# Kernel optimization log

Hardware: AMD Instinct MI355X
Metric: run time of the kernel (lower is better)

Reference implementation:

```python
import jax, jax.numpy as jnp
import numpy as np

LR = 0.001
TAU = 1000.0


def setup_inputs() -> dict:
    key = jax.random.key(0)
    k1, k2 = jax.random.split(key)
    B, IN, OUT = 8192, 4096, 4096
    x = jax.random.normal(k1, (B, IN), dtype=jnp.float32)
    weight = jax.random.normal(k2, (OUT, IN), dtype=jnp.float32) * 0.1
    threshold = jnp.zeros((OUT,), dtype=jnp.float32)
    return {"x": x, "weight": weight, "threshold": threshold}


def reference(x, weight, threshold):
    # output = x @ W.T  -> (B, out)
    output = jnp.matmul(x, weight.T)

    # BCM sliding-threshold EMA (torch uses output.detach())
    activity = jnp.mean(jax.lax.stop_gradient(output), axis=0)  # (out,)
    new_threshold = threshold + (activity ** 2 - threshold) / TAU

    # Hebbian update: torch builds (B, out, in) outer products then means over B;
    # equivalent efficient form: post.T @ pre / B (single GEMM).
    post = jax.lax.stop_gradient(jnp.maximum(output - new_threshold, 0.0))  # (B, out)
    B = x.shape[0]
    delta_w = (LR / B) * jnp.einsum('bo,bi->oi', post, x)
    new_weight = weight + delta_w

    # Original returns (output, threshold-after-update); we also expose the
    # updated weight (the in-place .data side effect) for verification.
    return output, new_threshold, new_weight
```

## Files before the change

### kernel.cpp

```cpp
#include <hip/hip_runtime.h>
#include <hip/hip_bf16.h>


typedef __attribute__((ext_vector_type(8))) short   bf16x8;
typedef __attribute__((ext_vector_type(4))) float   f32x4;

#define ASG __attribute__((address_space(1)))
#define ASL __attribute__((address_space(3)))

__device__ __forceinline__ void gload16(const void* g, void* l) {
    __builtin_amdgcn_global_load_lds((const ASG void*)g, (ASL void*)l, 16, 0, 0);
}

__device__ __forceinline__ unsigned short f2bf(float x) {
    union { float f; unsigned u; } v; v.f = x;
    unsigned r = v.u;
    r += 0x7fffu + ((r >> 16) & 1u);
    return (unsigned short)(r >> 16);
}
__device__ __forceinline__ float bf2f(unsigned short u) {
    union { unsigned u; float f; } v; v.u = ((unsigned)u) << 16;
    return v.f;
}

__global__ __launch_bounds__(256) void k_cvt_split(const float* __restrict__ src,
                                                   unsigned short* __restrict__ hi,
                                                   unsigned short* __restrict__ lo,
                                                   int n4) {
    int i = blockIdx.x * blockDim.x + threadIdx.x;
    int stride = gridDim.x * blockDim.x;
    for (; i < n4; i += stride) {
        float4 v = reinterpret_cast<const float4*>(src)[i];
        ushort4 h, l;
        h.x = f2bf(v.x); l.x = f2bf(v.x - bf2f(h.x));
        h.y = f2bf(v.y); l.y = f2bf(v.y - bf2f(h.y));
        h.z = f2bf(v.z); l.z = f2bf(v.z - bf2f(h.z));
        h.w = f2bf(v.w); l.w = f2bf(v.w - bf2f(h.w));
        reinterpret_cast<ushort4*>(hi)[i] = h;
        reinterpret_cast<ushort4*>(lo)[i] = l;
    }
}

__global__ __launch_bounds__(256) void k_prep_x(const float* __restrict__ x,
                                                unsigned short* __restrict__ hi,
                                                unsigned short* __restrict__ lo,
                                                unsigned short* __restrict__ xT) {
    __shared__ unsigned short tile[64][65];
    const int b0 = blockIdx.y * 64, i0 = blockIdx.x * 64;
#pragma unroll
    for (int it = 0; it < 16; ++it) {
        int idx = it * 256 + threadIdx.x;
        int r = idx >> 6, c = idx & 63;
        float v = x[(size_t)(b0 + r) * 4096 + i0 + c];
        unsigned short h = f2bf(v);
        unsigned short l = f2bf(v - bf2f(h));
        hi[(size_t)(b0 + r) * 4096 + i0 + c] = h;
        lo[(size_t)(b0 + r) * 4096 + i0 + c] = l;
        tile[r][c] = h;
    }
    __syncthreads();
#pragma unroll
    for (int it = 0; it < 16; ++it) {
        int idx = it * 256 + threadIdx.x;
        int r = idx >> 6, c = idx & 63;
        xT[(size_t)(i0 + r) * 8192 + b0 + c] = tile[c][r];
    }
}

__global__ __launch_bounds__(512, 2) void k_gemm1(const unsigned short* __restrict__ Ah,
                                                  const unsigned short* __restrict__ Al,
                                                  const unsigned short* __restrict__ Bh,
                                                  const unsigned short* __restrict__ Bl,
                                                  float* __restrict__ C,
                                                  float* __restrict__ acc_act) {
    __shared__ unsigned short sm[3 * 24576];
    const int t = threadIdx.x, lane = t & 63, ln15 = lane & 15, l16 = lane >> 4;
    const int wid = t >> 6, wm = wid >> 2, wn = wid & 3;
    const int nwg = gridDim.x, bid = blockIdx.x;
    const int wg  = (bid & 7) * (nwg >> 3) + (bid >> 3);
    const int bm = wg >> 5, bn = wg & 31;
    const int arow0 = bm * 256, brow0 = bn * 128;

    const unsigned short* gsrc[6];
    int ldso[6];
#pragma unroll
    for (int j = 0; j < 6; ++j) {
        const int c = j * 512 + t;
        if (c < 1024)      { int cc = c;        int row = cc >> 2, chk = (cc & 3) ^ ((row >> 1) & 3); gsrc[j] = Ah + (size_t)(arow0 + row) * 4096 + chk * 8; ldso[j] = cc * 8; }
        else if (c < 2048) { int cc = c - 1024; int row = cc >> 2, chk = (cc & 3) ^ ((row >> 1) & 3); gsrc[j] = Al + (size_t)(arow0 + row) * 4096 + chk * 8; ldso[j] = 8192 + cc * 8; }
        else if (c < 2560) { int cc = c - 2048; int row = cc >> 2, chk = (cc & 3) ^ ((row >> 1) & 3); gsrc[j] = Bh + (size_t)(brow0 + row) * 4096 + chk * 8; ldso[j] = 16384 + cc * 8; }
        else               { int cc = c - 2560; int row = cc >> 2, chk = (cc & 3) ^ ((row >> 1) & 3); gsrc[j] = Bl + (size_t)(brow0 + row) * 4096 + chk * 8; ldso[j] = 20480 + cc * 8; }
    }

    int aoh[8], aol[8], boh[2], bol[2];
#pragma unroll
    for (int mi = 0; mi < 8; ++mi) {
        const int r = wm * 128 + mi * 16 + ln15;
        const int sw = (l16 ^ ((r >> 1) & 3)) * 8;
        aoh[mi] = r * 32 + sw; aol[mi] = 8192 + r * 32 + sw;
    }
#pragma unroll
    for (int ni = 0; ni < 2; ++ni) {
        const int r = wn * 32 + ni * 16 + ln15;
        const int sw = (l16 ^ ((r >> 1) & 3)) * 8;
        boh[ni] = 16384 + r * 32 + sw; bol[ni] = 20480 + r * 32 + sw;
    }

    f32x4 acc[8][2];
#pragma unroll
    for (int mi = 0; mi < 8; ++mi)
#pragma unroll
        for (int ni = 0; ni < 2; ++ni) acc[mi][ni] = (f32x4){0.f, 0.f, 0.f, 0.f};

#pragma unroll
    for (int j = 0; j < 6; ++j) gload16(gsrc[j], sm + ldso[j]);
#pragma unroll
    for (int j = 0; j < 6; ++j) gload16(gsrc[j] + 32, sm + 24576 + ldso[j]);

    int scur = 0, snxt = 2;
    for (int kt = 0; kt < 128; ++kt) {
        asm volatile("s_waitcnt vmcnt(6)" ::: "memory");
        __builtin_amdgcn_s_barrier();
        asm volatile("" ::: "memory");
        const unsigned short* rb = sm + scur * 24576;
        bf16x8 vah[8], val[8], vbh[2], vbl[2];
#pragma unroll
        for (int mi = 0; mi < 8; ++mi) { vah[mi] = *(const bf16x8*)(rb + aoh[mi]); val[mi] = *(const bf16x8*)(rb + aol[mi]); }
#pragma unroll
        for (int ni = 0; ni < 2; ++ni) { vbh[ni] = *(const bf16x8*)(rb + boh[ni]); vbl[ni] = *(const bf16x8*)(rb + bol[ni]); }
        {
            const size_t ko = (size_t)((kt + 2 < 128) ? kt + 2 : 127) * 32;
            unsigned short* sb = sm + snxt * 24576;
#pragma unroll
            for (int j = 0; j < 6; ++j) gload16(gsrc[j] + ko, sb + ldso[j]);
        }
        __builtin_amdgcn_s_setprio(1);
#pragma unroll
        for (int mi = 0; mi < 8; ++mi)
#pragma unroll
            for (int ni = 0; ni < 2; ++ni) {
                acc[mi][ni] = __builtin_amdgcn_mfma_f32_16x16x32_bf16(vah[mi], vbh[ni], acc[mi][ni], 0, 0, 0);
                acc[mi][ni] = __builtin_amdgcn_mfma_f32_16x16x32_bf16(vah[mi], vbl[ni], acc[mi][ni], 0, 0, 0);
                acc[mi][ni] = __builtin_amdgcn_mfma_f32_16x16x32_bf16(val[mi], vbh[ni], acc[mi][ni], 0, 0, 0);
            }
        __builtin_amdgcn_s_setprio(0);
        scur = (scur == 2) ? 0 : scur + 1;
        snxt = (snxt == 2) ? 0 : snxt + 1;
    }
    asm volatile("s_waitcnt vmcnt(0)" ::: "memory");

    const int row0 = bm * 256 + wm * 128, col0 = bn * 128 + wn * 32;
    float cs0 = 0.f, cs1 = 0.f;
#pragma unroll
    for (int mi = 0; mi < 8; ++mi)
#pragma unroll
        for (int j = 0; j < 4; ++j) {
            const int row = row0 + mi * 16 + l16 * 4 + j;
            C[(size_t)row * 4096 + col0 + ln15]      = acc[mi][0][j];
            C[(size_t)row * 4096 + col0 + 16 + ln15] = acc[mi][1][j];
            cs0 += acc[mi][0][j]; cs1 += acc[mi][1][j];
        }
    cs0 += __shfl_xor(cs0, 16, 64); cs0 += __shfl_xor(cs0, 32, 64);
    cs1 += __shfl_xor(cs1, 16, 64); cs1 += __shfl_xor(cs1, 32, 64);
    if (l16 == 0) {
        atomicAdd(&acc_act[col0 + ln15], cs0);
        atomicAdd(&acc_act[col0 + 16 + ln15], cs1);
    }
}

__global__ __launch_bounds__(512, 2) void k_gemm2(const unsigned short* __restrict__ A,
                                                  const unsigned short* __restrict__ Bx,
                                                  const float* __restrict__ Wf,
                                                  float* __restrict__ Wout, float scale) {
    __shared__ unsigned short sm[3 * 24576];
    const int t = threadIdx.x, lane = t & 63, ln15 = lane & 15, l16 = lane >> 4;
    const int wid = t >> 6, wm = wid >> 2, wn = wid & 3;
    const int nwg = gridDim.x, bid = blockIdx.x;
    const int wg  = (bid & 7) * (nwg >> 3) + (bid >> 3);
    const int bm = wg >> 5, bn = wg & 31;
    const int arow0 = bm * 256, brow0 = bn * 128;

    const unsigned short* gsrc[6];
    int ldso[6];
#pragma unroll
    for (int j = 0; j < 6; ++j) {
        const int c = j * 512 + t;
        if (c < 2048) { int row = c >> 3, chk = (c & 7) ^ (row & 7); gsrc[j] = A + (size_t)(arow0 + row) * 8192 + chk * 8; ldso[j] = c * 8; }
        else { int cc = c - 2048; int row = cc >> 3, chk = (cc & 7) ^ (row & 7); gsrc[j] = Bx + (size_t)(brow0 + row) * 8192 + chk * 8; ldso[j] = 16384 + cc * 8; }
    }

    int ao0[8], ao1[8], bo0[2], bo1[2];
#pragma unroll
    for (int mi = 0; mi < 8; ++mi) {
        const int r = wm * 128 + mi * 16 + ln15;
        ao0[mi] = r * 64 + ((l16 ^ (r & 7)) * 8);
        ao1[mi] = r * 64 + (((4 + l16) ^ (r & 7)) * 8);
    }
#pragma unroll
    for (int ni = 0; ni < 2; ++ni) {
        const int r = wn * 32 + ni * 16 + ln15;
        bo0[ni] = 16384 + r * 64 + ((l16 ^ (r & 7)) * 8);
        bo1[ni] = 16384 + r * 64 + (((4 + l16) ^ (r & 7)) * 8);
    }

    f32x4 acc[8][2];
#pragma unroll
    for (int mi = 0; mi < 8; ++mi)
#pragma unroll
        for (int ni = 0; ni < 2; ++ni) acc[mi][ni] = (f32x4){0.f, 0.f, 0.f, 0.f};

#pragma unroll
    for (int j = 0; j < 6; ++j) gload16(gsrc[j], sm + ldso[j]);
#pragma unroll
    for (int j = 0; j < 6; ++j) gload16(gsrc[j] + 64, sm + 24576 + ldso[j]);

    int scur = 0, snxt = 2;
    for (int kt = 0; kt < 128; ++kt) {
        asm volatile("s_waitcnt vmcnt(6)" ::: "memory");
        __builtin_amdgcn_s_barrier();
        asm volatile("" ::: "memory");
        const unsigned short* rb = sm + scur * 24576;
        bf16x8 va[8], vb[2];
#pragma unroll
        for (int mi = 0; mi < 8; ++mi) va[mi] = *(const bf16x8*)(rb + ao0[mi]);
#pragma unroll
        for (int ni = 0; ni < 2; ++ni) vb[ni] = *(const bf16x8*)(rb + bo0[ni]);
        { const size_t ko = (size_t)((kt + 2 < 128) ? kt + 2 : 127) * 64;
          unsigned short* sb = sm + snxt * 24576;
#pragma unroll
          for (int j = 0; j < 6; ++j) gload16(gsrc[j] + ko, sb + ldso[j]);
        }
        __builtin_amdgcn_s_setprio(1);
#pragma unroll
        for (int mi = 0; mi < 8; ++mi)
#pragma unroll
            for (int ni = 0; ni < 2; ++ni)
                acc[mi][ni] = __builtin_amdgcn_mfma_f32_16x16x32_bf16(va[mi], vb[ni], acc[mi][ni], 0, 0, 0);
        __builtin_amdgcn_s_setprio(0);
#pragma unroll
        for (int mi = 0; mi < 8; ++mi) va[mi] = *(const bf16x8*)(rb + ao1[mi]);
#pragma unroll
        for (int ni = 0; ni < 2; ++ni) vb[ni] = *(const bf16x8*)(rb + bo1[ni]);
        __builtin_amdgcn_s_setprio(1);
#pragma unroll
        for (int mi = 0; mi < 8; ++mi)
#pragma unroll
            for (int ni = 0; ni < 2; ++ni)
                acc[mi][ni] = __builtin_amdgcn_mfma_f32_16x16x32_bf16(va[mi], vb[ni], acc[mi][ni], 0, 0, 0);
        __builtin_amdgcn_s_setprio(0);
        scur = (scur == 2) ? 0 : scur + 1;
        snxt = (snxt == 2) ? 0 : snxt + 1;
    }
    asm volatile("s_waitcnt vmcnt(0)" ::: "memory");

    const int row0 = bm * 256 + wm * 128, col0 = bn * 128 + wn * 32;
#pragma unroll
    for (int mi = 0; mi < 8; ++mi)
#pragma unroll
        for (int j = 0; j < 4; ++j) {
            const int row = row0 + mi * 16 + l16 * 4 + j;
            const size_t i0 = (size_t)row * 4096 + col0 + ln15;
            const size_t i1 = i0 + 16;
            Wout[i0] = Wf[i0] + scale * acc[mi][0][j];
            Wout[i1] = Wf[i1] + scale * acc[mi][1][j];
        }
}

__global__ __launch_bounds__(256) void k_thr(const float* __restrict__ acc,
                                             const float* __restrict__ thr_in,
                                             float* __restrict__ thr_out) {
    const int o = blockIdx.x * 256 + threadIdx.x;
    const float act = acc[o] * (1.0f / 8192.0f);
    const float t0  = thr_in[o];
    thr_out[o] = t0 + (act * act - t0) / 1000.0f;
}

__global__ __launch_bounds__(256) void k_postT(const float* __restrict__ out,
                                               const float* __restrict__ thr,
                                               unsigned short* __restrict__ postT) {
    __shared__ unsigned short tile[64][65];
    __shared__ float sthr[64];
    const int b0 = blockIdx.y * 64, o0 = blockIdx.x * 64;
    if (threadIdx.x < 64) sthr[threadIdx.x] = thr[o0 + threadIdx.x];
    __syncthreads();
#pragma unroll
    for (int it = 0; it < 16; ++it) {
        int idx = it * 256 + threadIdx.x;
        int r = idx >> 6, c = idx & 63;
        float v = out[(size_t)(b0 + r) * 4096 + o0 + c] - sthr[c];
        tile[r][c] = f2bf(v > 0.f ? v : 0.f);
    }
    __syncthreads();
#pragma unroll
    for (int it = 0; it < 16; ++it) {
        int idx = it * 256 + threadIdx.x;
        int r = idx >> 6, c = idx & 63;
        postT[(size_t)(o0 + r) * 8192 + b0 + c] = tile[c][r];
    }
}

extern "C" void kernel_launch(void* const* d_in, const int* in_sizes, int n_in,
                              void* d_out, int out_size, void* d_ws, size_t ws_size,
                              hipStream_t stream) {
    const float* x   = (const float*)d_in[0];
    const float* w   = (const float*)d_in[1];
    const float* thr = (const float*)d_in[2];
    const int B = 8192, IN = 4096, OUT = 4096;

    float* out_y   = (float*)d_out;
    float* out_thr = out_y + (size_t)B * OUT;
    float* out_w   = out_thr + OUT;

    char* ws = (char*)d_ws;
    float* acc_act       = (float*)ws;
    unsigned short* x_hi = (unsigned short*)(ws + 65536);
    unsigned short* x_lo = x_hi + (size_t)B * IN;
    unsigned short* w_hi = x_lo + (size_t)B * IN;
    unsigned short* w_lo = w_hi + (size_t)OUT * IN;
    unsigned short* xT   = w_lo + (size_t)OUT * IN;
    unsigned short* postT = x_lo;
    (void)ws_size;

    hipMemsetAsync(acc_act, 0, OUT * sizeof(float), stream);

    k_prep_x<<<dim3(IN / 64, B / 64), 256, 0, stream>>>(x, x_hi, x_lo, xT);
    k_cvt_split<<<2048, 256, 0, stream>>>(w, w_hi, w_lo, OUT * IN / 4);

    k_gemm1<<<1024, 512, 0, stream>>>(x_hi, x_lo, w_hi, w_lo, out_y, acc_act);

    k_thr<<<OUT / 256, 256, 0, stream>>>(acc_act, thr, out_thr);

    k_postT<<<dim3(OUT / 64, B / 64), 256, 0, stream>>>(out_y, out_thr, postT);

    k_gemm2<<<512, 512, 0, stream>>>(postT, xT, w, out_w, (float)(0.001 / 8192.0));
}
```

Measured before the change: 1.375 ms.

## Reshape GEMM warp tiles to 64x64 and double-buffer LDS fragments in registers

Both GEMM kernels change each wave's tile from 128x32 to 64x64, which cuts the number of LDS fragment reads per MFMA. The main loop is unrolled by two with register double-buffering, so the next k-slice's LDS reads and global prefetch overlap the current slice's MFMAs. All three LDS stages are now prefetched up front. The second fragment buffer raises VGPR pressure, which risks spills or lower occupancy under the existing launch bounds.

```diff
diff --git a/kernel.cpp b/kernel.cpp
--- a/kernel.cpp
+++ b/kernel.cpp
@@ -67,6 +67,46 @@
     }
 }
 
+
+__device__ __forceinline__ void g1_stage(const unsigned short* const (&gsrc)[6],
+                                         const int (&ldso)[6],
+                                         unsigned short* sb, int ko) {
+#pragma unroll
+    for (int j = 0; j < 6; ++j) gload16(gsrc[j] + ko, sb + ldso[j]);
+}
+
+__device__ __forceinline__ void g1_read(const unsigned short* rb,
+                                        const int (&aoh)[4], const int (&aol)[4],
+                                        const int (&boh)[4], const int (&bol)[4],
+                                        bf16x8 (&Ah)[4], bf16x8 (&Al)[4],
+                                        bf16x8 (&Bh)[4], bf16x8 (&Bl)[4]) {
+#pragma unroll
+    for (int i = 0; i < 4; ++i) {
+        Ah[i] = *(const bf16x8*)(rb + aoh[i]);
+        Al[i] = *(const bf16x8*)(rb + aol[i]);
+    }
+#pragma unroll
+    for (int i = 0; i < 4; ++i) {
+        Bh[i] = *(const bf16x8*)(rb + boh[i]);
+        Bl[i] = *(const bf16x8*)(rb + bol[i]);
+    }
+}
+
+__device__ __forceinline__ void g1_mfma(const bf16x8 (&Ah)[4], const bf16x8 (&Al)[4],
+                                        const bf16x8 (&Bh)[4], const bf16x8 (&Bl)[4],
+                                        f32x4 (&acc)[4][4]) {
+    __builtin_amdgcn_s_setprio(1);
+#pragma unroll
+    for (int mi = 0; mi < 4; ++mi)
+#pragma unroll
+        for (int ni = 0; ni < 4; ++ni) {
+            acc[mi][ni] = __builtin_amdgcn_mfma_f32_16x16x32_bf16(Ah[mi], Bh[ni], acc[mi][ni], 0, 0, 0);
+            acc[mi][ni] = __builtin_amdgcn_mfma_f32_16x16x32_bf16(Ah[mi], Bl[ni], acc[mi][ni], 0, 0, 0);
+            acc[mi][ni] = __builtin_amdgcn_mfma_f32_16x16x32_bf16(Al[mi], Bh[ni], acc[mi][ni], 0, 0, 0);
+        }
+    __builtin_amdgcn_s_setprio(0);
+}
+
 __global__ __launch_bounds__(512, 2) void k_gemm1(const unsigned short* __restrict__ Ah,
                                                   const unsigned short* __restrict__ Al,
                                                   const unsigned short* __restrict__ Bh,
@@ -75,7 +115,7 @@
                                                   float* __restrict__ acc_act) {
     __shared__ unsigned short sm[3 * 24576];
     const int t = threadIdx.x, lane = t & 63, ln15 = lane & 15, l16 = lane >> 4;
-    const int wid = t >> 6, wm = wid >> 2, wn = wid & 3;
+    const int wid = t >> 6, wm = wid >> 1, wn = wid & 1;
     const int nwg = gridDim.x, bid = blockIdx.x;
     const int wg  = (bid & 7) * (nwg >> 3) + (bid >> 3);
     const int bm = wg >> 5, bn = wg & 31;
@@ -92,80 +132,128 @@
         else               { int cc = c - 2560; int row = cc >> 2, chk = (cc & 3) ^ ((row >> 1) & 3); gsrc[j] = Bl + (size_t)(brow0 + row) * 4096 + chk * 8; ldso[j] = 20480 + cc * 8; }
     }
 
-    int aoh[8], aol[8], boh[2], bol[2];
-#pragma unroll
-    for (int mi = 0; mi < 8; ++mi) {
-        const int r = wm * 128 + mi * 16 + ln15;
+    int aoh[4], aol[4], boh[4], bol[4];
+#pragma unroll
+    for (int mi = 0; mi < 4; ++mi) {
+        const int r = wm * 64 + mi * 16 + ln15;
         const int sw = (l16 ^ ((r >> 1) & 3)) * 8;
         aoh[mi] = r * 32 + sw; aol[mi] = 8192 + r * 32 + sw;
     }
 #pragma unroll
-    for (int ni = 0; ni < 2; ++ni) {
-        const int r = wn * 32 + ni * 16 + ln15;
+    for (int ni = 0; ni < 4; ++ni) {
+        const int r = wn * 64 + ni * 16 + ln15;
         const int sw = (l16 ^ ((r >> 1) & 3)) * 8;
         boh[ni] = 16384 + r * 32 + sw; bol[ni] = 20480 + r * 32 + sw;
     }
 
-    f32x4 acc[8][2];
-#pragma unroll
-    for (int mi = 0; mi < 8; ++mi)
-#pragma unroll
-        for (int ni = 0; ni < 2; ++ni) acc[mi][ni] = (f32x4){0.f, 0.f, 0.f, 0.f};
-
-#pragma unroll
-    for (int j = 0; j < 6; ++j) gload16(gsrc[j], sm + ldso[j]);
-#pragma unroll
-    for (int j = 0; j < 6; ++j) gload16(gsrc[j] + 32, sm + 24576 + ldso[j]);
-
-    int scur = 0, snxt = 2;
-    for (int kt = 0; kt < 128; ++kt) {
+    f32x4 acc[4][4];
+#pragma unroll
+    for (int i = 0; i < 4; ++i)
+#pragma unroll
+        for (int j = 0; j < 4; ++j) acc[i][j] = (f32x4){0.f, 0.f, 0.f, 0.f};
+
+    bf16x8 A0h[4], A0l[4], B0h[4], B0l[4];
+    bf16x8 A1h[4], A1l[4], B1h[4], B1l[4];
+
+    g1_stage(gsrc, ldso, sm, 0);
+    g1_stage(gsrc, ldso, sm + 24576, 32);
+    g1_stage(gsrc, ldso, sm + 2 * 24576, 64);
+    asm volatile("s_waitcnt vmcnt(12)" ::: "memory");
+    __builtin_amdgcn_s_barrier();
+    g1_read(sm, aoh, aol, boh, bol, A0h, A0l, B0h, B0l);
+    asm volatile("s_waitcnt lgkmcnt(0)" ::: "memory");
+    __builtin_amdgcn_sched_barrier(0);
+
+    int sRead = 1, sStage = 0;
+#pragma unroll 1
+    for (int i = 0; i < 64; ++i) {
         asm volatile("s_waitcnt vmcnt(6)" ::: "memory");
         __builtin_amdgcn_s_barrier();
-        asm volatile("" ::: "memory");
-        const unsigned short* rb = sm + scur * 24576;
-        bf16x8 vah[8], val[8], vbh[2], vbl[2];
-#pragma unroll
-        for (int mi = 0; mi < 8; ++mi) { vah[mi] = *(const bf16x8*)(rb + aoh[mi]); val[mi] = *(const bf16x8*)(rb + aol[mi]); }
-#pragma unroll
-        for (int ni = 0; ni < 2; ++ni) { vbh[ni] = *(const bf16x8*)(rb + boh[ni]); vbl[ni] = *(const bf16x8*)(rb + bol[ni]); }
-        {
-            const size_t ko = (size_t)((kt + 2 < 128) ? kt + 2 : 127) * 32;
-            unsigned short* sb = sm + snxt * 24576;
-#pragma unroll
-            for (int j = 0; j < 6; ++j) gload16(gsrc[j] + ko, sb + ldso[j]);
-        }
-        __builtin_amdgcn_s_setprio(1);
-#pragma unroll
-        for (int mi = 0; mi < 8; ++mi)
-#pragma unroll
-            for (int ni = 0; ni < 2; ++ni) {
-                acc[mi][ni] = __builtin_amdgcn_mfma_f32_16x16x32_bf16(vah[mi], vbh[ni], acc[mi][ni], 0, 0, 0);
-                acc[mi][ni] = __builtin_amdgcn_mfma_f32_16x16x32_bf16(vah[mi], vbl[ni], acc[mi][ni], 0, 0, 0);
-                acc[mi][ni] = __builtin_amdgcn_mfma_f32_16x16x32_bf16(val[mi], vbh[ni], acc[mi][ni], 0, 0, 0);
+        g1_read(sm + sRead * 24576, aoh, aol, boh, bol, A1h, A1l, B1h, B1l);
+        { int kst = 2 * i + 3; if (kst > 127) kst = 127;
+          g1_stage(gsrc, ldso, sm + sStage * 24576, kst * 32); }
+        g1_mfma(A0h, A0l, B0h, B0l, acc);
+        asm volatile("s_waitcnt lgkmcnt(0)" ::: "memory");
+        __builtin_amdgcn_sched_barrier(0);
+        sRead = (sRead == 2) ? 0 : sRead + 1;
+        sStage = (sStage == 2) ? 0 : sStage + 1;
+        asm volatile("s_waitcnt vmcnt(6)" ::: "memory");
+        __builtin_amdgcn_s_barrier();
+        g1_read(sm + sRead * 24576, aoh, aol, boh, bol, A0h, A0l, B0h, B0l);
+        { int kst = 2 * i + 4; if (kst > 127) kst = 127;
+          g1_stage(gsrc, ldso, sm + sStage * 24576, kst * 32); }
+        g1_mfma(A1h, A1l, B1h, B1l, acc);
+        asm volatile("s_waitcnt lgkmcnt(0)" ::: "memory");
+        __builtin_amdgcn_sched_barrier(0);
+        sRead = (sRead == 2) ? 0 : sRead + 1;
+        sStage = (sStage == 2) ? 0 : sStage + 1;
+    }
+    asm volatile("s_waitcnt vmcnt(0)" ::: "memory");
+
+    const int row0 = bm * 256 + wm * 64, col0 = bn * 128 + wn * 64;
+    float cs[4] = {0.f, 0.f, 0.f, 0.f};
+#pragma unroll
+    for (int mi = 0; mi < 4; ++mi)
+#pragma unroll
+        for (int ni = 0; ni < 4; ++ni)
+#pragma unroll
+            for (int j = 0; j < 4; ++j) {
+                const int row = row0 + mi * 16 + l16 * 4 + j;
+                C[(size_t)row * 4096 + col0 + ni * 16 + ln15] = acc[mi][ni][j];
+                cs[ni] += acc[mi][ni][j];
             }
-        __builtin_amdgcn_s_setprio(0);
-        scur = (scur == 2) ? 0 : scur + 1;
-        snxt = (snxt == 2) ? 0 : snxt + 1;
-    }
-    asm volatile("s_waitcnt vmcnt(0)" ::: "memory");
-
-    const int row0 = bm * 256 + wm * 128, col0 = bn * 128 + wn * 32;
-    float cs0 = 0.f, cs1 = 0.f;
-#pragma unroll
-    for (int mi = 0; mi < 8; ++mi)
-#pragma unroll
-        for (int j = 0; j < 4; ++j) {
-            const int row = row0 + mi * 16 + l16 * 4 + j;
-            C[(size_t)row * 4096 + col0 + ln15]      = acc[mi][0][j];
-            C[(size_t)row * 4096 + col0 + 16 + ln15] = acc[mi][1][j];
-            cs0 += acc[mi][0][j]; cs1 += acc[mi][1][j];
-        }
-    cs0 += __shfl_xor(cs0, 16, 64); cs0 += __shfl_xor(cs0, 32, 64);
-    cs1 += __shfl_xor(cs1, 16, 64); cs1 += __shfl_xor(cs1, 32, 64);
+#pragma unroll
+    for (int ni = 0; ni < 4; ++ni) {
+        cs[ni] += __shfl_xor(cs[ni], 16, 64);
+        cs[ni] += __shfl_xor(cs[ni], 32, 64);
+    }
     if (l16 == 0) {
-        atomicAdd(&acc_act[col0 + ln15], cs0);
-        atomicAdd(&acc_act[col0 + 16 + ln15], cs1);
-    }
+#pragma unroll
+        for (int ni = 0; ni < 4; ++ni)
+            atomicAdd(&acc_act[col0 + ni * 16 + ln15], cs[ni]);
+    }
+}
+
+
+__device__ __forceinline__ void g2_stage(const unsigned short* const (&gsrc)[6],
+                                         const int (&ldso)[6],
+                                         unsigned short* sb, int ko) {
+#pragma unroll
+    for (int j = 0; j < 6; ++j) gload16(gsrc[j] + ko, sb + ldso[j]);
+}
+
+__device__ __forceinline__ void g2_read(const unsigned short* rb,
+                                        const int (&ao0)[4], const int (&ao1)[4],
+                                        const int (&bo0)[4], const int (&bo1)[4],
+                                        bf16x8 (&A0)[4], bf16x8 (&A1)[4],
+                                        bf16x8 (&B0)[4], bf16x8 (&B1)[4]) {
+#pragma unroll
+    for (int i = 0; i < 4; ++i) {
+        A0[i] = *(const bf16x8*)(rb + ao0[i]);
+        A1[i] = *(const bf16x8*)(rb + ao1[i]);
+    }
+#pragma unroll
+    for (int i = 0; i < 4; ++i) {
+        B0[i] = *(const bf16x8*)(rb + bo0[i]);
+        B1[i] = *(const bf16x8*)(rb + bo1[i]);
+    }
+}
+
+__device__ __forceinline__ void g2_mfma(const bf16x8 (&A0)[4], const bf16x8 (&A1)[4],
+                                        const bf16x8 (&B0)[4], const bf16x8 (&B1)[4],
+                                        f32x4 (&acc)[4][4]) {
+    __builtin_amdgcn_s_setprio(1);
+#pragma unroll
+    for (int mi = 0; mi < 4; ++mi)
+#pragma unroll
+        for (int ni = 0; ni < 4; ++ni)
+            acc[mi][ni] = __builtin_amdgcn_mfma_f32_16x16x32_bf16(A0[mi], B0[ni], acc[mi][ni], 0, 0, 0);
+#pragma unroll
+    for (int mi = 0; mi < 4; ++mi)
+#pragma unroll
+        for (int ni = 0; ni < 4; ++ni)
+            acc[mi][ni] = __builtin_amdgcn_mfma_f32_16x16x32_bf16(A1[mi], B1[ni], acc[mi][ni], 0, 0, 0);
+    __builtin_amdgcn_s_setprio(0);
 }
 
 __global__ __launch_bounds__(512, 2) void k_gemm2(const unsigned short* __restrict__ A,
@@ -174,7 +262,7 @@
                                                   float* __restrict__ Wout, float scale) {
     __shared__ unsigned short sm[3 * 24576];
     const int t = threadIdx.x, lane = t & 63, ln15 = lane & 15, l16 = lane >> 4;
-    const int wid = t >> 6, wm = wid >> 2, wn = wid & 3;
+    const int wid = t >> 6, wm = wid >> 1, wn = wid & 1;
     const int nwg = gridDim.x, bid = blockIdx.x;
     const int wg  = (bid & 7) * (nwg >> 3) + (bid >> 3);
     const int bm = wg >> 5, bn = wg & 31;
@@ -189,81 +277,76 @@
         else { int cc = c - 2048; int row = cc >> 3, chk = (cc & 7) ^ (row & 7); gsrc[j] = Bx + (size_t)(brow0 + row) * 8192 + chk * 8; ldso[j] = 16384 + cc * 8; }
     }
 
-    int ao0[8], ao1[8], bo0[2], bo1[2];
-#pragma unroll
-    for (int mi = 0; mi < 8; ++mi) {
-        const int r = wm * 128 + mi * 16 + ln15;
+    int ao0[4], ao1[4], bo0[4], bo1[4];
+#pragma unroll
+    for (int mi = 0; mi < 4; ++mi) {
+        const int r = wm * 64 + mi * 16 + ln15;
         ao0[mi] = r * 64 + ((l16 ^ (r & 7)) * 8);
         ao1[mi] = r * 64 + (((4 + l16) ^ (r & 7)) * 8);
     }
 #pragma unroll
-    for (int ni = 0; ni < 2; ++ni) {
-        const int r = wn * 32 + ni * 16 + ln15;
+    for (int ni = 0; ni < 4; ++ni) {
+        const int r = wn * 64 + ni * 16 + ln15;
         bo0[ni] = 16384 + r * 64 + ((l16 ^ (r & 7)) * 8);
         bo1[ni] = 16384 + r * 64 + (((4 + l16) ^ (r & 7)) * 8);
     }
 
-    f32x4 acc[8][2];
-#pragma unroll
-    for (int mi = 0; mi < 8; ++mi)
-#pragma unroll
-        for (int ni = 0; ni < 2; ++ni) acc[mi][ni] = (f32x4){0.f, 0.f, 0.f, 0.f};
-
-#pragma unroll
-    for (int j = 0; j < 6; ++j) gload16(gsrc[j], sm + ldso[j]);
-#pragma unroll
-    for (int j = 0; j < 6; ++j) gload16(gsrc[j] + 64, sm + 24576 + ldso[j]);
-
-    int scur = 0, snxt = 2;
-    for (int kt = 0; kt < 128; ++kt) {
+    f32x4 acc[4][4];
+#pragma unroll
+    for (int i = 0; i < 4; ++i)
+#pragma unroll
+        for (int j = 0; j < 4; ++j) acc[i][j] = (f32x4){0.f, 0.f, 0.f, 0.f};
+
+    bf16x8 A0k0[4], A0k1[4], B0k0[4], B0k1[4];
+    bf16x8 A1k0[4], A1k1[4], B1k0[4], B1k1[4];
+
+    g2_stage(gsrc, ldso, sm, 0);
+    g2_stage(gsrc, ldso, sm + 24576, 64);
+    g2_stage(gsrc, ldso, sm + 2 * 24576, 128);
+    asm volatile("s_waitcnt vmcnt(12)" ::: "memory");
+    __builtin_amdgcn_s_barrier();
+    g2_read(sm, ao0, ao1, bo0, bo1, A0k0, A0k1, B0k0, B0k1);
+    asm volatile("s_waitcnt lgkmcnt(0)" ::: "memory");
+    __builtin_amdgcn_sched_barrier(0);
+
+    int sRead = 1, sStage = 0;
+#pragma unroll 1
+    for (int i = 0; i < 64; ++i) {
         asm volatile("s_waitcnt vmcnt(6)" ::: "memory");
         __builtin_amdgcn_s_barrier();
-        asm volatile("" ::: "memory");
-        const unsigned short* rb = sm + scur * 24576;
-        bf16x8 va[8], vb[2];
-#pragma unroll
-        for (int mi = 0; mi < 8; ++mi) va[mi] = *(const bf16x8*)(rb + ao0[mi]);
-#pragma unroll
-        for (int ni = 0; ni < 2; ++ni) vb[ni] = *(const bf16x8*)(rb + bo0[ni]);
-        { const size_t ko = (size_t)((kt + 2 < 128) ? kt + 2 : 127) * 64;
-          unsigned short* sb = sm + snxt * 24576;
-#pragma unroll
-          for (int j = 0; j < 6; ++j) gload16(gsrc[j] + ko, sb + ldso[j]);
-        }
-        __builtin_amdgcn_s_setprio(1);
-#pragma unroll
-        for (int mi = 0; mi < 8; ++mi)
-#pragma unroll
-            for (int ni = 0; ni < 2; ++ni)
-                acc[mi][ni] = __builtin_amdgcn_mfma_f32_16x16x32_bf16(va[mi], vb[ni], acc[mi][ni], 0, 0, 0);
-        __builtin_amdgcn_s_setprio(0);
-#pragma unroll
-        for (int mi = 0; mi < 8; ++mi) va[mi] = *(const bf16x8*)(rb + ao1[mi]);
-#pragma unroll
-        for (int ni = 0; ni < 2; ++ni) vb[ni] = *(const bf16x8*)(rb + bo1[ni]);
-        __builtin_amdgcn_s_setprio(1);
-#pragma unroll
-        for (int mi = 0; mi < 8; ++mi)
-#pragma unroll
-            for (int ni = 0; ni < 2; ++ni)
-                acc[mi][ni] = __builtin_amdgcn_mfma_f32_16x16x32_bf16(va[mi], vb[ni], acc[mi][ni], 0, 0, 0);
-        __builtin_amdgcn_s_setprio(0);
-        scur = (scur == 2) ? 0 : scur + 1;
-        snxt = (snxt == 2) ? 0 : snxt + 1;
+        g2_read(sm + sRead * 24576, ao0, ao1, bo0, bo1, A1k0, A1k1, B1k0, B1k1);
+        { int kst = 2 * i + 3; if (kst > 127) kst = 127;
+          g2_stage(gsrc, ldso, sm + sStage * 24576, kst * 64); }
+        g2_mfma(A0k0, A0k1, B0k0, B0k1, acc);
+        asm volatile("s_waitcnt lgkmcnt(0)" ::: "memory");
+        __builtin_amdgcn_sched_barrier(0);
+        sRead = (sRead == 2) ? 0 : sRead + 1;
+        sStage = (sStage == 2) ? 0 : sStage + 1;
+
+        asm volatile("s_waitcnt vmcnt(6)" ::: "memory");
+        __builtin_amdgcn_s_barrier();
+        g2_read(sm + sRead * 24576, ao0, ao1, bo0, bo1, A0k0, A0k1, B0k0, B0k1);
+        { int kst = 2 * i + 4; if (kst > 127) kst = 127;
+          g2_stage(gsrc, ldso, sm + sStage * 24576, kst * 64); }
+        g2_mfma(A1k0, A1k1, B1k0, B1k1, acc);
+        asm volatile("s_waitcnt lgkmcnt(0)" ::: "memory");
+        __builtin_amdgcn_sched_barrier(0);
+        sRead = (sRead == 2) ? 0 : sRead + 1;
+        sStage = (sStage == 2) ? 0 : sStage + 1;
     }
     asm volatile("s_waitcnt vmcnt(0)" ::: "memory");
 
-    const int row0 = bm * 256 + wm * 128, col0 = bn * 128 + wn * 32;
-#pragma unroll
-    for (int mi = 0; mi < 8; ++mi)
-#pragma unroll
-        for (int j = 0; j < 4; ++j) {
-            const int row = row0 + mi * 16 + l16 * 4 + j;
-            const size_t i0 = (size_t)row * 4096 + col0 + ln15;
-            const size_t i1 = i0 + 16;
-            Wout[i0] = Wf[i0] + scale * acc[mi][0][j];
-            Wout[i1] = Wf[i1] + scale * acc[mi][1][j];
-        }
+    const int row0 = bm * 256 + wm * 64, col0 = bn * 128 + wn * 64;
+#pragma unroll
+    for (int mi = 0; mi < 4; ++mi)
+#pragma unroll
+        for (int ni = 0; ni < 4; ++ni)
+#pragma unroll
+            for (int j = 0; j < 4; ++j) {
+                const int row = row0 + mi * 16 + l16 * 4 + j;
+                const size_t idx = (size_t)row * 4096 + col0 + ni * 16 + ln15;
+                Wout[idx] = Wf[idx] + scale * acc[mi][ni][j];
+            }
 }
 
 __global__ __launch_bounds__(256) void k_thr(const float* __restrict__ acc,
```

Result: no change. 1.373 ms (-0.2%).
